# Performance work log

Measured on AMD Instinct MI355X. Metric: run time of the kernel, lower is better.

Reference implementation:

```python
import jax, jax.numpy as jnp
import numpy as np

N = 100_000   # nodes
E = 3_200_000 # edges
G = 512       # graphs in batch
H = 64        # hidden dim
C = 7         # num classes


def setup_inputs() -> dict:
    key = jax.random.key(0)
    ks = jax.random.split(key, 8)
    x = jax.random.normal(ks[0], (N, 1), dtype=jnp.float32)
    edge_index = jax.random.randint(ks[1], (2, E), 0, N, dtype=jnp.int32)
    batch = jnp.sort(jax.random.randint(ks[2], (N,), 0, G, dtype=jnp.int32))
    W1 = jax.random.normal(ks[3], (1, H), dtype=jnp.float32) / np.sqrt(1.0)
    b1 = jnp.zeros((H,), jnp.float32)
    W2 = jax.random.normal(ks[4], (H, H), dtype=jnp.float32) / np.sqrt(H)
    b2 = jnp.zeros((H,), jnp.float32)
    fW1 = jax.random.normal(ks[5], (H, 32), dtype=jnp.float32) / np.sqrt(H)
    fb1 = jnp.zeros((32,), jnp.float32)
    fW2 = jax.random.normal(ks[6], (32, C), dtype=jnp.float32) / np.sqrt(32.0)
    fb2 = jnp.zeros((C,), jnp.float32)
    return {"x": x, "edge_index": edge_index, "batch": batch,
            "W1": W1, "b1": b1, "W2": W2, "b2": b2,
            "fW1": fW1, "fb1": fb1, "fW2": fW2, "fb2": fb2}


def reference(x, edge_index, batch, W1, b1, W2, b2, fW1, fb1, fW2, fb2):
    # GCNConv with self-loops and symmetric normalization (PyG defaults).
    src, dst = edge_index[0], edge_index[1]
    loop = jnp.arange(N, dtype=src.dtype)
    s = jnp.concatenate([src, loop])  # [E+N]
    d = jnp.concatenate([dst, loop])
    deg = jax.ops.segment_sum(jnp.ones(s.shape, jnp.float32), d, num_segments=N)
    dis = jnp.where(deg > 0, jax.lax.rsqrt(jnp.maximum(deg, 1.0)), 0.0)
    norm = dis[s] * dis[d]  # [E+N]

    def gcn(h, W, b):
        h = h @ W                                   # [N, out]
        msg = norm[:, None] * h[s]                  # gather + scale
        return jax.ops.segment_sum(msg, d, num_segments=N) + b

    # Dropout is identity in eval/reference mode.
    h = jax.nn.relu(gcn(x, W1, b1))
    h = jax.nn.relu(gcn(h, W2, b2))

    # global_mean_pool over graph assignment `batch`
    cnt = jax.ops.segment_sum(jnp.ones((N,), jnp.float32), batch, num_segments=G)
    pooled = jax.ops.segment_sum(h, batch, num_segments=G) / jnp.maximum(cnt, 1.0)[:, None]

    h = jax.nn.relu(pooled @ fW1 + fb1)
    return h @ fW2 + fb2  # [G, C] logits
```

## Files before the change

### kernel.cpp

```cpp
#include <hip/hip_runtime.h>

#define N_NODES 100000
#define N_EDGES 3200000
#define G_GRAPHS 512
#define HDIM 64
#define CBSH 11
#define CBN 2048
#define NCB ((N_NODES + CBN - 1) / CBN)
#define EPW 4096
#define NWG ((N_EDGES + EPW - 1) / EPW)
#define EPT (EPW / 256)
#define SPL 16
#define WPS ((NWG + SPL - 1) / SPL)
#define MAXROWS 25

__global__ void kprep_small(const float* __restrict__ W1, const float* __restrict__ b1,
                            float* __restrict__ dt, int* __restrict__ meta,
                            float* __restrict__ pw1, float* __restrict__ pb1,
                            int* __restrict__ pdidx, int* __restrict__ kperm_g,
                            int* __restrict__ rank_g) {
    __shared__ float ts[HDIM], srt[HDIM];
    __shared__ int isnew[HDIM], bW[HDIM], kpermS[HDIM], rankS[HDIM];
    int j = threadIdx.x;
    float w1 = W1[j], bb = b1[j];
    float tj = (w1 != 0.f) ? (-bb / w1) : -1e30f;
    ts[j] = tj;
    bW[j] = (bb != 0.f) ? 1 : 0;
    __syncthreads();
    int r = 0;
    for (int i = 0; i < HDIM; ++i) {
        float ti = ts[i];
        if (ti < tj || (ti == tj && i < j)) r++;
    }
    srt[r] = tj;
    kpermS[r] = j;
    __syncthreads();
    isnew[r] = (r == 0) || (srt[r] != srt[r - 1]);
    __syncthreads();
    int didx = 0;
    for (int q = 0; q <= r; ++q) didx += isnew[q];
    didx -= 1;
    if (isnew[r]) dt[didx] = srt[r];
    rankS[j] = didx;
    __syncthreads();
    if (j == 0) {
        int nd = 0, nw = 0;
        for (int q = 0; q < HDIM; ++q) { nd += isnew[q]; nw |= bW[q]; }
        meta[0] = nd; meta[1] = nw;
    }
    int pj = kpermS[j];
    pw1[j] = W1[pj]; pb1[j] = b1[pj]; pdidx[j] = rankS[pj];
    kperm_g[j] = kpermS[j];
    rank_g[j] = rankS[j];
}

__global__ void kprep_tab(const float* __restrict__ W1, const float* __restrict__ b1,
                          const float* __restrict__ W2, const int* __restrict__ kperm_g,
                          const int* __restrict__ rank_g, const int* __restrict__ meta,
                          float* __restrict__ w2p, float* __restrict__ tabs) {
    int i = blockIdx.x * blockDim.x + threadIdx.x;
    int nd = meta[0];
    if (i < HDIM * HDIM) {
        int r = i >> 6, j = i & 63;
        w2p[i] = W2[kperm_g[r] * HDIM + j];
    }
    if (nd <= 6 && i < (1 + 4 * nd) * HDIM) {
        int r = i >> 6, j = i & 63;
        float acc = 0.f;
        if (r == 0) {
            for (int jj = 0; jj < HDIM; ++jj)
                if (W1[jj] == 0.f) acc += fmaxf(b1[jj], 0.f) * W2[jj * HDIM + j];
        } else {
            int q = (r - 1) >> 2, c = (r - 1) & 3;
            for (int jj = 0; jj < HDIM; ++jj) {
                if (rank_g[jj] != q) continue;
                float w1 = W1[jj], bb = b1[jj];
                float wr = W2[jj * HDIM + j];
                if      (c == 0 && w1 > 0.f) acc += w1 * wr;
                else if (c == 1 && w1 < 0.f) acc += w1 * wr;
                else if (c == 2 && w1 > 0.f) acc += bb * wr;
                else if (c == 3 && w1 < 0.f) acc += bb * wr;
            }
        }
        tabs[i] = acc;
    }
}

__global__ void kzero(int* __restrict__ deg, float* __restrict__ q,
                      float* __restrict__ pool, int* __restrict__ cnt,
                      float* __restrict__ histA, float* __restrict__ histW,
                      const int* __restrict__ meta) {
    int nd = meta[0], needW = meta[1];
    size_t tid = (size_t)blockIdx.x * blockDim.x + threadIdx.x;
    size_t stride = (size_t)gridDim.x * blockDim.x;
    for (size_t i = tid; i < N_NODES; i += stride) { deg[i] = 0; q[i] = 0.f; }
    for (size_t i = tid; i < G_GRAPHS * HDIM; i += stride) pool[i] = 0.f;
    for (size_t i = tid; i < G_GRAPHS; i += stride) cnt[i] = 0;
    if (nd <= 6) {
        size_t nh = (size_t)(nd + 1) * N_NODES;
        for (size_t i = tid; i < nh; i += stride) histA[i] = 0.f;
        if (needW) for (size_t i = tid; i < nh; i += stride) histW[i] = 0.f;
    }
}

__global__ __launch_bounds__(256) void kB2(const int* __restrict__ src,
                                           const int* __restrict__ dst,
                                           unsigned* __restrict__ sorted,
                                           int* __restrict__ wgcnt,
                                           int* __restrict__ wgpre) {
    __shared__ int hist[NCB];
    __shared__ int basep[NCB];
    __shared__ unsigned sbuf[EPW];
    int tid = threadIdx.x;
    int w = blockIdx.x;
    int e0 = w * EPW;
    int ecnt = min(EPW, N_EDGES - e0);
    if (tid < NCB) hist[tid] = 0;
    __syncthreads();
    int dreg[EPT], sreg[EPT];
    #pragma unroll
    for (int t = 0; t < EPT; ++t) {
        int i = t * 256 + tid;
        if (i < ecnt) {
            int d = dst[e0 + i];
            dreg[t] = d; sreg[t] = src[e0 + i];
            atomicAdd(&hist[d >> CBSH], 1);
        } else dreg[t] = -1;
    }
    __syncthreads();
    if (tid < 64) {
        int h = (tid < NCB) ? hist[tid] : 0;
        int v = h;
        #pragma unroll
        for (int off = 1; off < 64; off <<= 1) {
            int uu = __shfl_up(v, off, 64);
            if (tid >= off) v += uu;
        }
        if (tid < NCB) {
            basep[tid] = v - h;
            wgcnt[w * NCB + tid] = h;
            wgpre[w * NCB + tid] = v - h;
        }
    }
    __syncthreads();
    #pragma unroll
    for (int t = 0; t < EPT; ++t) {
        int d = dreg[t];
        if (d >= 0) {
            int b = d >> CBSH;
            int pos = atomicAdd(&basep[b], 1);
            sbuf[pos] = ((unsigned)sreg[t] << CBSH) | (unsigned)(d & (CBN - 1));
        }
    }
    __syncthreads();
    for (int i = tid; i < ecnt; i += 256)
        sorted[e0 + i] = sbuf[i];
}

#define FOR_RUNS(BODY)                                                        \
    {                                                                         \
        int wv = tid >> 6, ln = tid & 63;                                     \
        int w0 = sp * WPS, w1e = min(w0 + WPS, NWG);                          \
        for (int w = w0 + wv; w < w1e; w += 4) {                              \
            int st = w * EPW + wgpre[w * NCB + b];                            \
            int cb = wgcnt[w * NCB + b];                                      \
            for (int i = ln; i < cb; i += 64) { unsigned ww = sorted[st + i]; BODY } \
        }                                                                     \
    }

__global__ __launch_bounds__(256) void kdeg2(const unsigned* __restrict__ sorted,
                                             const int* __restrict__ wgcnt,
                                             const int* __restrict__ wgpre,
                                             int* __restrict__ deg) {
    __shared__ int dcnt[CBN];
    int b = blockIdx.x / SPL, sp = blockIdx.x % SPL, tid = threadIdx.x;
    for (int i = tid; i < CBN; i += 256) dcnt[i] = 0;
    __syncthreads();
    FOR_RUNS( atomicAdd(&dcnt[ww & (CBN - 1)], 1); )
    __syncthreads();
    int nb = b * CBN;
    for (int i = tid; i < CBN; i += 256) {
        int c = dcnt[i];
        if (c && nb + i < N_NODES) atomicAdd(&deg[nb + i], c);
    }
}

__global__ void k2_dis(const int* __restrict__ deg, const float* __restrict__ x,
                       float* __restrict__ dis, float* __restrict__ u) {
    int n = blockIdx.x * blockDim.x + threadIdx.x;
    if (n < N_NODES) {
        float d = rsqrtf((float)(deg[n] + 1));
        dis[n] = d;
        u[n] = d * x[n];
    }
}

__global__ __launch_bounds__(256) void kq3(const unsigned* __restrict__ sorted,
                                           const int* __restrict__ wgcnt,
                                           const int* __restrict__ wgpre,
                                           const float* __restrict__ u,
                                           float* __restrict__ q) {
    __shared__ float qL[CBN];
    int b = blockIdx.x / SPL, sp = blockIdx.x % SPL, tid = threadIdx.x;
    for (int i = tid; i < CBN; i += 256) qL[i] = 0.f;
    __syncthreads();
    FOR_RUNS( atomicAdd(&qL[ww & (CBN - 1)], u[ww >> CBSH]); )
    __syncthreads();
    int nb = b * CBN;
    for (int i = tid; i < CBN; i += 256) {
        float v = qL[i];
        if (v != 0.f && nb + i < N_NODES) atomicAdd(&q[nb + i], v);
    }
}

__global__ void k3b(const int* __restrict__ deg, const float* __restrict__ x,
                    const float* __restrict__ dis, const float* __restrict__ q,
                    float2* __restrict__ ad) {
    int n = blockIdx.x * blockDim.x + threadIdx.x;
    if (n < N_NODES) {
        float d = dis[n];
        ad[n] = make_float2(d * q[n] + x[n] / (float)(deg[n] + 1), d);
    }
}

template<int LO, int HI, int PLANES>
__global__ __launch_bounds__(256) void khist3t(const unsigned* __restrict__ sorted,
                                               const int* __restrict__ wgcnt,
                                               const int* __restrict__ wgpre,
                                               const float2* __restrict__ ad,
                                               const float* __restrict__ dt,
                                               const int* __restrict__ meta,
                                               float* __restrict__ histA,
                                               float* __restrict__ histW) {
    __shared__ float bA[PLANES * CBN];
    __shared__ float dtS[8];
    int nd = meta[0], needW = meta[1];
    if (nd < LO || nd > HI) return;
    int b = blockIdx.x / SPL, sp = blockIdx.x % SPL, tid = threadIdx.x;
    if (tid < 8) dtS[tid] = (tid < nd) ? dt[tid] : 3.4e38f;
    int nb = b * CBN;
    int nparts = 1 + (needW ? 1 : 0);
    for (int part = 0; part < nparts; ++part) {
        for (int i = tid; i < (nd + 1) * CBN; i += 256) bA[i] = 0.f;
        __syncthreads();
        FOR_RUNS(
            float2 t = ad[ww >> CBSH];
            float a = t.x;
            int k = 0;
            _Pragma("unroll")
            for (int qq = 0; qq < HI; ++qq) k += (dtS[qq] < a) ? 1 : 0;
            atomicAdd(&bA[k * CBN + (ww & (CBN - 1))], part ? t.y : t.y * a);
        )
        __syncthreads();
        float* H = part ? histW : histA;
        for (int k = 0; k <= nd; ++k)
            for (int i = tid; i < CBN; i += 256) {
                float v = bA[k * CBN + i];
                if (v != 0.f && nb + i < N_NODES)
                    atomicAdd(&H[(size_t)k * N_NODES + nb + i], v);
            }
        __syncthreads();
    }
}

__global__ __launch_bounds__(256) void knode(
        const float* __restrict__ histA, const float* __restrict__ histW,
        const int* __restrict__ meta, const float* __restrict__ dt,
        const float* __restrict__ tabs,
        const float* __restrict__ pw1, const float* __restrict__ pb1,
        const float* __restrict__ w2p,
        const float2* __restrict__ ad, const float* __restrict__ b2,
        const int* __restrict__ batch,
        const unsigned* __restrict__ sorted, const int* __restrict__ wgcnt,
        const int* __restrict__ wgpre,
        float* __restrict__ pool, int* __restrict__ cnt) {
    __shared__ float h2s[HDIM * 65];
    __shared__ float tabL[MAXROWS * HDIM];
    __shared__ float dtS[8];
    int tid = threadIdx.x;
    int nl = tid & 63, cg = tid >> 6;
    int n0 = blockIdx.x * 64;
    int nvalid = min(64, N_NODES - n0);
    int n = n0 + min(nl, nvalid - 1);
    int nd = meta[0], needW = meta[1];
    float2 adn = ad[n];
    float a = adn.x, d = adn.y;
    int c16 = cg * 16;

    if (nd <= 6) {
        int nrows = 1 + 4 * nd;
        for (int i = tid; i < nrows * HDIM; i += 256) tabL[i] = tabs[i];
        if (tid < nd) dtS[tid] = dt[tid];
        __syncthreads();
        float TA = 0.f, TW = 0.f;
        for (int bq = 0; bq <= nd; ++bq) {
            TA += histA[(size_t)bq * N_NODES + n];
            if (needW) TW += histW[(size_t)bq * N_NODES + n];
        }
        int k = 0;
        for (int q = 0; q < nd; ++q) k += (dtS[q] < a) ? 1 : 0;
        float z[16];
        #pragma unroll
        for (int t = 0; t < 16; ++t) z[t] = b2[c16 + t];
        float d2 = d * d;
        float cC = d * TW + d2;
        #pragma unroll
        for (int t = 0; t < 16; ++t) z[t] += cC * tabL[c16 + t];
        float run = 0.f, runW = 0.f;
        for (int q = 0; q < nd; ++q) {
            run += histA[(size_t)q * N_NODES + n];
            if (needW) runW += histW[(size_t)q * N_NODES + n];
            bool act = (q < k);
            float cWp = d * (TA - run) + (act ? d2 * a : 0.f);
            float cWm = d * run + (act ? 0.f : d2 * a);
            float cBp = d * (TW - runW) + (act ? d2 : 0.f);
            float cBm = d * runW + (act ? 0.f : d2);
            int base = (1 + 4 * q) * HDIM + c16;
            #pragma unroll
            for (int t = 0; t < 16; ++t)
                z[t] += cWp * tabL[base + t] + cWm * tabL[base + HDIM + t]
                      + cBp * tabL[base + 2 * HDIM + t] + cBm * tabL[base + 3 * HDIM + t];
        }
        #pragma unroll
        for (int t = 0; t < 16; ++t) h2s[nl * 65 + c16 + t] = fmaxf(z[t], 0.f);
    } else {
        float areg[HDIM];
        #pragma unroll
        for (int jj = 0; jj < HDIM; ++jj) areg[jj] = 0.f;
        int b = n >> CBSH;
        int myld = n & (CBN - 1);
        for (int w = 0; w < NWG; ++w) {
            int st = w * EPW + wgpre[w * NCB + b];
            int cb = wgcnt[w * NCB + b];
            for (int i = 0; i < cb; ++i) {
                unsigned ww = sorted[st + i];
                if ((int)(ww & (CBN - 1)) == myld) {
                    float2 t = ad[ww >> CBSH];
                    #pragma unroll
                    for (int jj = 0; jj < HDIM; ++jj)
                        areg[jj] += t.y * fmaxf(t.x * pw1[jj] + pb1[jj], 0.f);
                }
            }
        }
        #pragma unroll
        for (int jj = 0; jj < HDIM; ++jj)
            areg[jj] = d * areg[jj] + d * d * fmaxf(a * pw1[jj] + pb1[jj], 0.f);
        float z[16];
        #pragma unroll
        for (int t = 0; t < 16; ++t) z[t] = b2[c16 + t];
        for (int jj = 0; jj < HDIM; ++jj) {
            float av = areg[jj];
            #pragma unroll
            for (int t = 0; t < 16; ++t) z[t] += av * w2p[jj * HDIM + c16 + t];
        }
        #pragma unroll
        for (int t = 0; t < 16; ++t) h2s[nl * 65 + c16 + t] = fmaxf(z[t], 0.f);
    }

    __syncthreads();
    int i0 = cg * 16, i1 = min(i0 + 16, nvalid);
    float accP = 0.f; int gcur = -1, runC = 0;
    for (int i = i0; i < i1; ++i) {
        int g = batch[n0 + i];
        float v = h2s[i * 65 + nl];
        if (g != gcur) {
            if (gcur >= 0) {
                atomicAdd(&pool[(size_t)gcur * HDIM + nl], accP);
                if (nl == 0) atomicAdd(&cnt[gcur], runC);
            }
            gcur = g; accP = 0.f; runC = 0;
        }
        accP += v; ++runC;
    }
    if (gcur >= 0) {
        atomicAdd(&pool[(size_t)gcur * HDIM + nl], accP);
        if (nl == 0) atomicAdd(&cnt[gcur], runC);
    }
}

__global__ void k7_mlp(const float* __restrict__ pool, const int* __restrict__ cnt,
                       const float* __restrict__ fW1, const float* __restrict__ fb1,
                       const float* __restrict__ fW2, const float* __restrict__ fb2,
                       float* __restrict__ out) {
    __shared__ float p[HDIM];
    __shared__ float tt[32];
    int g = blockIdx.x;
    int tid = threadIdx.x;
    float c = fmaxf((float)cnt[g], 1.f);
    p[tid] = pool[g * HDIM + tid] / c;
    __syncthreads();
    if (tid < 32) {
        float acc = fb1[tid];
        #pragma unroll
        for (int j = 0; j < HDIM; ++j) acc += p[j] * fW1[j * 32 + tid];
        tt[tid] = fmaxf(acc, 0.f);
    }
    __syncthreads();
    if (tid < 7) {
        float acc = fb2[tid];
        #pragma unroll
        for (int i = 0; i < 32; ++i) acc += tt[i] * fW2[i * 7 + tid];
        out[g * 7 + tid] = acc;
    }
}

__global__ void kf1_deg(const int* __restrict__ dst, int* __restrict__ deg) {
    int e = blockIdx.x * blockDim.x + threadIdx.x;
    if (e < N_EDGES) atomicAdd(&deg[dst[e]], 1);
}
__global__ void kf2_dis(const int* __restrict__ deg, const float* __restrict__ x,
                        float* __restrict__ dis, float* __restrict__ agg1) {
    int n = blockIdx.x * blockDim.x + threadIdx.x;
    if (n < N_NODES) {
        float d = (float)(deg[n] + 1);
        dis[n] = rsqrtf(d);
        agg1[n] = x[n] / d;
    }
}
__global__ void kf3_agg1(const int* __restrict__ src, const int* __restrict__ dst,
                         const float* __restrict__ dis, const float* __restrict__ x,
                         float* __restrict__ agg1) {
    int e = blockIdx.x * blockDim.x + threadIdx.x;
    if (e < N_EDGES) {
        int s = src[e], d = dst[e];
        atomicAdd(&agg1[d], dis[s] * dis[d] * x[s]);
    }
}
__global__ void kf4_agg2init(const float* __restrict__ agg1, const float* __restrict__ dis,
                             const float* __restrict__ W1, const float* __restrict__ b1,
                             float* __restrict__ agg2) {
    int i = blockIdx.x * blockDim.x + threadIdx.x;
    if (i < N_NODES * HDIM) {
        int n = i >> 6, j = i & 63;
        float h = fmaxf(agg1[n] * W1[j] + b1[j], 0.f);
        float r = dis[n];
        agg2[i] = r * r * h;
    }
}
__global__ void kf5_edge(const int* __restrict__ src, const int* __restrict__ dst,
                         const float* __restrict__ dis, const float* __restrict__ agg1,
                         const float* __restrict__ W1, const float* __restrict__ b1,
                         float* __restrict__ agg2) {
    int t = blockIdx.x * blockDim.x + threadIdx.x;
    int e = t >> 6, j = t & 63;
    if (e < N_EDGES) {
        int s = src[e], d = dst[e];
        float w = dis[s] * dis[d];
        float h = fmaxf(agg1[s] * W1[j] + b1[j], 0.f);
        atomicAdd(&agg2[d * HDIM + j], w * h);
    }
}
__global__ void kf6_pool(const float* __restrict__ agg2, const float* __restrict__ W2,
                         const float* __restrict__ b2, const int* __restrict__ batch,
                         float* __restrict__ pool, int* __restrict__ cnt) {
    __shared__ float w2s[HDIM * HDIM];
    int tid = threadIdx.x;
    for (int i = tid; i < HDIM * HDIM; i += blockDim.x) w2s[i] = W2[i];
    __syncthreads();
    int lane = tid & 63, wid = tid >> 6;
    int nwaves = gridDim.x * 4;
    for (int n = blockIdx.x * 4 + wid; n < N_NODES; n += nwaves) {
        float av  = agg2[n * HDIM + lane];
        float acc = b2[lane];
        #pragma unroll
        for (int k = 0; k < HDIM; ++k)
            acc += __shfl(av, k, 64) * w2s[k * HDIM + lane];
        acc = fmaxf(acc, 0.f);
        int g = batch[n];
        atomicAdd(&pool[g * HDIM + lane], acc);
        if (lane == 0) atomicAdd(&cnt[g], 1);
    }
}

extern "C" void kernel_launch(void* const* d_in, const int* in_sizes, int n_in,
                              void* d_out, int out_size, void* d_ws, size_t ws_size,
                              hipStream_t stream) {
    const float* x    = (const float*)d_in[0];
    const int*   ei   = (const int*)  d_in[1];
    const int*   batch= (const int*)  d_in[2];
    const float* W1   = (const float*)d_in[3];
    const float* b1   = (const float*)d_in[4];
    const float* W2   = (const float*)d_in[5];
    const float* b2   = (const float*)d_in[6];
    const float* fW1  = (const float*)d_in[7];
    const float* fb1  = (const float*)d_in[8];
    const float* fW2  = (const float*)d_in[9];
    const float* fb2  = (const float*)d_in[10];
    const int* src = ei;
    const int* dst = ei + N_EDGES;
    float* out = (float*)d_out;

    size_t off = 0;
    auto take = [&](size_t bytes) { size_t o = off; off = (off + bytes + 255) & ~(size_t)255; return o; };
    char* base = (char*)d_ws;
    int*     deg   = (int*)     (base + take((size_t)N_NODES * 4));
    float*   pool  = (float*)   (base + take((size_t)G_GRAPHS * HDIM * 4));
    int*     cnt   = (int*)     (base + take((size_t)G_GRAPHS * 4));
    float*   dis   = (float*)   (base + take((size_t)N_NODES * 4));
    float*   u     = (float*)   (base + take((size_t)N_NODES * 4));
    float*   q     = (float*)   (base + take((size_t)N_NODES * 4));
    float2*  ad    = (float2*)  (base + take((size_t)N_NODES * 8));
    float*   dt    = (float*)   (base + take(HDIM * 4));
    int*     meta  = (int*)     (base + take(64));
    float*   pw1   = (float*)   (base + take(HDIM * 4));
    float*   pb1   = (float*)   (base + take(HDIM * 4));
    int*     pdidx = (int*)     (base + take(HDIM * 4));
    int*     kperm_g = (int*)   (base + take(HDIM * 4));
    int*     rank_g  = (int*)   (base + take(HDIM * 4));
    float*   w2p   = (float*)   (base + take(HDIM * HDIM * 4));
    float*   tabs  = (float*)   (base + take((size_t)MAXROWS * HDIM * 4));
    int*     wgcnt = (int*)     (base + take((size_t)NWG * NCB * 4));
    int*     wgpre = (int*)     (base + take((size_t)NWG * NCB * 4));
    size_t sorted_off = off;
    unsigned* sorted = (unsigned*)(base + take((size_t)N_EDGES * 4));
    float*   histA = (float*)   (base + take((size_t)7 * N_NODES * 4));
    float*   histW = (float*)   (base + take((size_t)7 * N_NODES * 4));
    size_t need_fast = off;

    if (ws_size >= need_fast) {
        kprep_small<<<1, HDIM, 0, stream>>>(W1, b1, dt, meta, pw1, pb1, pdidx, kperm_g, rank_g);
        kprep_tab<<<16, 256, 0, stream>>>(W1, b1, W2, kperm_g, rank_g, meta, w2p, tabs);
        kzero <<<1024, 256, 0, stream>>>(deg, q, pool, cnt, histA, histW, meta);
        kB2   <<<NWG, 256, 0, stream>>>(src, dst, sorted, wgcnt, wgpre);
        kdeg2 <<<NCB * SPL, 256, 0, stream>>>(sorted, wgcnt, wgpre, deg);
        k2_dis<<<(N_NODES + 255) / 256, 256, 0, stream>>>(deg, x, dis, u);
        kq3   <<<NCB * SPL, 256, 0, stream>>>(sorted, wgcnt, wgpre, u, q);
        k3b   <<<(N_NODES + 255) / 256, 256, 0, stream>>>(deg, x, dis, q, ad);
        khist3t<0, 1, 2><<<NCB * SPL, 256, 0, stream>>>(sorted, wgcnt, wgpre, ad, dt, meta, histA, histW);
        khist3t<2, 3, 4><<<NCB * SPL, 256, 0, stream>>>(sorted, wgcnt, wgpre, ad, dt, meta, histA, histW);
        khist3t<4, 6, 7><<<NCB * SPL, 256, 0, stream>>>(sorted, wgcnt, wgpre, ad, dt, meta, histA, histW);
        knode <<<(N_NODES + 63) / 64, 256, 0, stream>>>(histA, histW, meta, dt, tabs,
                                                        pw1, pb1, w2p, ad, b2, batch,
                                                        sorted, wgcnt, wgpre, pool, cnt);
        k7_mlp<<<G_GRAPHS, 64, 0, stream>>>(pool, cnt, fW1, fb1, fW2, fb2, out);
    } else {
        float* agg1 = u;
        float* agg2 = (float*)(base + sorted_off);
        hipMemsetAsync(deg, 0, (size_t)N_NODES * 4, stream);
        hipMemsetAsync(pool, 0, (size_t)G_GRAPHS * HDIM * 4 + 1024, stream);
        kf1_deg<<<(N_EDGES + 255) / 256, 256, 0, stream>>>(dst, deg);
        kf2_dis<<<(N_NODES + 255) / 256, 256, 0, stream>>>(deg, x, dis, agg1);
        kf3_agg1<<<(N_EDGES + 255) / 256, 256, 0, stream>>>(src, dst, dis, x, agg1);
        kf4_agg2init<<<(N_NODES * HDIM + 255) / 256, 256, 0, stream>>>(agg1, dis, W1, b1, agg2);
        int k5_blocks = (int)(((long long)N_EDGES * HDIM + 255) / 256);
        kf5_edge<<<k5_blocks, 256, 0, stream>>>(src, dst, dis, agg1, W1, b1, agg2);
        kf6_pool<<<2048, 256, 0, stream>>>(agg2, W2, b2, batch, pool, cnt);
        k7_mlp<<<G_GRAPHS, 64, 0, stream>>>(pool, cnt, fW1, fb1, fW2, fb2, out);
    }
}
```

Baseline: 156.5 us.

## Merge prep kernels, vectorize edge bucketing, collapse histogram passes into two launches

Folds the two weight-preparation kernels into one 16-block kernel in which every block recomputes the threshold sort in shared memory, so the global permutation buffers disappear. The edge bucketing kernel now loads src/dst and stores sorted keys as uint4. The three histogram passes become two by widening the second template range. kzero no longer reads meta and always clears the full 7-row histA and histW arrays. This removes launches and global round trips but adds more zeroing traffic, redundant sort work per block, and more work per histogram pass.

```diff
diff --git a/kernel.cpp b/kernel.cpp
--- a/kernel.cpp
+++ b/kernel.cpp
@@ -14,55 +14,67 @@
 #define WPS ((NWG + SPL - 1) / SPL)
 #define MAXROWS 25
 
-__global__ void kprep_small(const float* __restrict__ W1, const float* __restrict__ b1,
-                            float* __restrict__ dt, int* __restrict__ meta,
-                            float* __restrict__ pw1, float* __restrict__ pb1,
-                            int* __restrict__ pdidx, int* __restrict__ kperm_g,
-                            int* __restrict__ rank_g) {
+__global__ __launch_bounds__(256) void kprep(const float* __restrict__ W1,
+                                             const float* __restrict__ b1,
+                                             const float* __restrict__ W2,
+                                             float* __restrict__ dt, int* __restrict__ meta,
+                                             float* __restrict__ pw1, float* __restrict__ pb1,
+                                             int* __restrict__ pdidx,
+                                             float* __restrict__ w2p, float* __restrict__ tabs) {
     __shared__ float ts[HDIM], srt[HDIM];
-    __shared__ int isnew[HDIM], bW[HDIM], kpermS[HDIM], rankS[HDIM];
-    int j = threadIdx.x;
-    float w1 = W1[j], bb = b1[j];
-    float tj = (w1 != 0.f) ? (-bb / w1) : -1e30f;
-    ts[j] = tj;
-    bW[j] = (bb != 0.f) ? 1 : 0;
-    __syncthreads();
-    int r = 0;
-    for (int i = 0; i < HDIM; ++i) {
-        float ti = ts[i];
-        if (ti < tj || (ti == tj && i < j)) r++;
-    }
-    srt[r] = tj;
-    kpermS[r] = j;
-    __syncthreads();
-    isnew[r] = (r == 0) || (srt[r] != srt[r - 1]);
-    __syncthreads();
-    int didx = 0;
-    for (int q = 0; q <= r; ++q) didx += isnew[q];
-    didx -= 1;
-    if (isnew[r]) dt[didx] = srt[r];
-    rankS[j] = didx;
-    __syncthreads();
-    if (j == 0) {
-        int nd = 0, nw = 0;
-        for (int q = 0; q < HDIM; ++q) { nd += isnew[q]; nw |= bW[q]; }
-        meta[0] = nd; meta[1] = nw;
-    }
-    int pj = kpermS[j];
-    pw1[j] = W1[pj]; pb1[j] = b1[pj]; pdidx[j] = rankS[pj];
-    kperm_g[j] = kpermS[j];
-    rank_g[j] = rankS[j];
-}
-
-__global__ void kprep_tab(const float* __restrict__ W1, const float* __restrict__ b1,
-                          const float* __restrict__ W2, const int* __restrict__ kperm_g,
-                          const int* __restrict__ rank_g, const int* __restrict__ meta,
-                          float* __restrict__ w2p, float* __restrict__ tabs) {
-    int i = blockIdx.x * blockDim.x + threadIdx.x;
-    int nd = meta[0];
+    __shared__ int isnew[HDIM], rr[HDIM], kpermS[HDIM], rankS[HDIM];
+    __shared__ int ndS;
+    int tid = threadIdx.x;
+    if (tid < HDIM) {
+        float w1 = W1[tid], bb = b1[tid];
+        ts[tid] = (w1 != 0.f) ? (-bb / w1) : -1e30f;
+    }
+    __syncthreads();
+    if (tid < HDIM) {
+        float tj = ts[tid];
+        int r = 0;
+        for (int i = 0; i < HDIM; ++i) {
+            float ti = ts[i];
+            if (ti < tj || (ti == tj && i < tid)) r++;
+        }
+        rr[tid] = r;
+        srt[r] = tj;
+        kpermS[r] = tid;
+    }
+    __syncthreads();
+    if (tid < HDIM) {
+        int r = rr[tid];
+        isnew[r] = (r == 0) || (srt[r] != srt[r - 1]);
+    }
+    __syncthreads();
+    if (tid < HDIM) {
+        int r = rr[tid];
+        int didx = 0;
+        for (int q = 0; q <= r; ++q) didx += isnew[q];
+        didx -= 1;
+        rankS[tid] = didx;
+        if (blockIdx.x == 0 && isnew[r]) dt[didx] = srt[r];
+    }
+    if (tid == 0) {
+        int nd = 0;
+        for (int q = 0; q < HDIM; ++q) nd += isnew[q];
+        ndS = nd;
+        if (blockIdx.x == 0) {
+            int nw = 0;
+            for (int q = 0; q < HDIM; ++q) nw |= (b1[q] != 0.f) ? 1 : 0;
+            meta[0] = nd; meta[1] = nw;
+        }
+    }
+    __syncthreads();
+    int nd = ndS;
+    if (blockIdx.x == 0 && tid < HDIM) {
+        int pj = kpermS[tid];
+        pw1[tid] = W1[pj]; pb1[tid] = b1[pj]; pdidx[tid] = rankS[pj];
+    }
+    int i = blockIdx.x * 256 + tid;
     if (i < HDIM * HDIM) {
         int r = i >> 6, j = i & 63;
-        w2p[i] = W2[kperm_g[r] * HDIM + j];
+        w2p[i] = W2[kpermS[r] * HDIM + j];
     }
     if (nd <= 6 && i < (1 + 4 * nd) * HDIM) {
         int r = i >> 6, j = i & 63;
@@ -73,7 +85,7 @@
         } else {
             int q = (r - 1) >> 2, c = (r - 1) & 3;
             for (int jj = 0; jj < HDIM; ++jj) {
-                if (rank_g[jj] != q) continue;
+                if (rankS[jj] != q) continue;
                 float w1 = W1[jj], bb = b1[jj];
                 float wr = W2[jj * HDIM + j];
                 if      (c == 0 && w1 > 0.f) acc += w1 * wr;
@@ -88,19 +100,14 @@
 
 __global__ void kzero(int* __restrict__ deg, float* __restrict__ q,
                       float* __restrict__ pool, int* __restrict__ cnt,
-                      float* __restrict__ histA, float* __restrict__ histW,
-                      const int* __restrict__ meta) {
-    int nd = meta[0], needW = meta[1];
+                      float* __restrict__ histA, float* __restrict__ histW) {
     size_t tid = (size_t)blockIdx.x * blockDim.x + threadIdx.x;
     size_t stride = (size_t)gridDim.x * blockDim.x;
     for (size_t i = tid; i < N_NODES; i += stride) { deg[i] = 0; q[i] = 0.f; }
     for (size_t i = tid; i < G_GRAPHS * HDIM; i += stride) pool[i] = 0.f;
     for (size_t i = tid; i < G_GRAPHS; i += stride) cnt[i] = 0;
-    if (nd <= 6) {
-        size_t nh = (size_t)(nd + 1) * N_NODES;
-        for (size_t i = tid; i < nh; i += stride) histA[i] = 0.f;
-        if (needW) for (size_t i = tid; i < nh; i += stride) histW[i] = 0.f;
-    }
+    size_t nh = (size_t)7 * N_NODES;
+    for (size_t i = tid; i < nh; i += stride) { histA[i] = 0.f; histW[i] = 0.f; }
 }
 
 __global__ __launch_bounds__(256) void kB2(const int* __restrict__ src,
@@ -118,14 +125,28 @@
     if (tid < NCB) hist[tid] = 0;
     __syncthreads();
     int dreg[EPT], sreg[EPT];
+    const uint4* dst4 = reinterpret_cast<const uint4*>(dst + e0);
+    const uint4* src4 = reinterpret_cast<const uint4*>(src + e0);
     #pragma unroll
-    for (int t = 0; t < EPT; ++t) {
-        int i = t * 256 + tid;
-        if (i < ecnt) {
-            int d = dst[e0 + i];
-            dreg[t] = d; sreg[t] = src[e0 + i];
-            atomicAdd(&hist[d >> CBSH], 1);
-        } else dreg[t] = -1;
+    for (int t = 0; t < EPT / 4; ++t) {
+        int v = t * 256 + tid;
+        if (v * 4 < ecnt) {
+            uint4 dv = dst4[v];
+            uint4 sv = src4[v];
+            int base = v * 4;
+            int d0 = (int)dv.x, d1 = (int)dv.y, d2 = (int)dv.z, d3 = (int)dv.w;
+            dreg[t*4+0] = (base+0 < ecnt) ? d0 : -1;
+            dreg[t*4+1] = (base+1 < ecnt) ? d1 : -1;
+            dreg[t*4+2] = (base+2 < ecnt) ? d2 : -1;
+            dreg[t*4+3] = (base+3 < ecnt) ? d3 : -1;
+            sreg[t*4+0] = (int)sv.x; sreg[t*4+1] = (int)sv.y;
+            sreg[t*4+2] = (int)sv.z; sreg[t*4+3] = (int)sv.w;
+            #pragma unroll
+            for (int k = 0; k < 4; ++k)
+                if (dreg[t*4+k] >= 0) atomicAdd(&hist[dreg[t*4+k] >> CBSH], 1);
+        } else {
+            dreg[t*4+0] = dreg[t*4+1] = dreg[t*4+2] = dreg[t*4+3] = -1;
+        }
     }
     __syncthreads();
     if (tid < 64) {
@@ -153,8 +174,11 @@
         }
     }
     __syncthreads();
-    for (int i = tid; i < ecnt; i += 256)
-        sorted[e0 + i] = sbuf[i];
+    uint4* out4 = reinterpret_cast<uint4*>(sorted + e0);
+    const uint4* sb4 = reinterpret_cast<const uint4*>(sbuf);
+    int nv4 = ecnt >> 2;
+    for (int i = tid; i < nv4; i += 256) out4[i] = sb4[i];
+    for (int i = (nv4 << 2) + tid; i < ecnt; i += 256) sorted[e0 + i] = sbuf[i];
 }
 
 #define FOR_RUNS(BODY)                                                        \
@@ -505,8 +529,6 @@
     float*   pw1   = (float*)   (base + take(HDIM * 4));
     float*   pb1   = (float*)   (base + take(HDIM * 4));
     int*     pdidx = (int*)     (base + take(HDIM * 4));
-    int*     kperm_g = (int*)   (base + take(HDIM * 4));
-    int*     rank_g  = (int*)   (base + take(HDIM * 4));
     float*   w2p   = (float*)   (base + take(HDIM * HDIM * 4));
     float*   tabs  = (float*)   (base + take((size_t)MAXROWS * HDIM * 4));
     int*     wgcnt = (int*)     (base + take((size_t)NWG * NCB * 4));
@@ -518,17 +540,15 @@
     size_t need_fast = off;
 
     if (ws_size >= need_fast) {
-        kprep_small<<<1, HDIM, 0, stream>>>(W1, b1, dt, meta, pw1, pb1, pdidx, kperm_g, rank_g);
-        kprep_tab<<<16, 256, 0, stream>>>(W1, b1, W2, kperm_g, rank_g, meta, w2p, tabs);
-        kzero <<<1024, 256, 0, stream>>>(deg, q, pool, cnt, histA, histW, meta);
+        kprep <<<16, 256, 0, stream>>>(W1, b1, W2, dt, meta, pw1, pb1, pdidx, w2p, tabs);
+        kzero <<<1024, 256, 0, stream>>>(deg, q, pool, cnt, histA, histW);
         kB2   <<<NWG, 256, 0, stream>>>(src, dst, sorted, wgcnt, wgpre);
         kdeg2 <<<NCB * SPL, 256, 0, stream>>>(sorted, wgcnt, wgpre, deg);
         k2_dis<<<(N_NODES + 255) / 256, 256, 0, stream>>>(deg, x, dis, u);
         kq3   <<<NCB * SPL, 256, 0, stream>>>(sorted, wgcnt, wgpre, u, q);
         k3b   <<<(N_NODES + 255) / 256, 256, 0, stream>>>(deg, x, dis, q, ad);
         khist3t<0, 1, 2><<<NCB * SPL, 256, 0, stream>>>(sorted, wgcnt, wgpre, ad, dt, meta, histA, histW);
-        khist3t<2, 3, 4><<<NCB * SPL, 256, 0, stream>>>(sorted, wgcnt, wgpre, ad, dt, meta, histA, histW);
-        khist3t<4, 6, 7><<<NCB * SPL, 256, 0, stream>>>(sorted, wgcnt, wgpre, ad, dt, meta, histA, histW);
+        khist3t<2, 6, 7><<<NCB * SPL, 256, 0, stream>>>(sorted, wgcnt, wgpre, ad, dt, meta, histA, histW);
         knode <<<(N_NODES + 63) / 64, 256, 0, stream>>>(histA, histW, meta, dt, tabs,
                                                         pw1, pb1, w2p, ad, b2, batch,
                                                         sorted, wgcnt, wgpre, pool, cnt);
```

Result: faster. 149.7 us (-4.3%).
